# Kernel optimization log

Hardware: AMD Instinct MI355X
Metric: run time of the kernel (lower is better)

## Reference

```python
import math
import jax, jax.numpy as jnp
import numpy as np

B, S, H = 2, 2048, 1024
NH = 16
HD = H // NH            # 64
ROT = int(HD * 0.25)    # 16
QKV_SLOTS = 1024
PROJ_SLOTS = 1024
FFN_SLOTS = 4096
EPS = 1e-5


def gelu_l2_norm(x, axis=-1):
    # F.gelu (exact erf) then L2-normalize and rescale by sqrt(dim)
    g = jax.nn.gelu(x, approximate=False)
    n = jnp.linalg.norm(g, ord=2, axis=axis, keepdims=True)
    return g / n * math.sqrt(g.shape[axis])


def layer_norm(x, w, b):
    mu = jnp.mean(x, axis=-1, keepdims=True)
    var = jnp.mean(jnp.square(x - mu), axis=-1, keepdims=True)
    return (x - mu) * jax.lax.rsqrt(var + EPS) * w + b


def pattention(x, key_tok, val_tok):
    # [.., in] @ [slots, in]^T -> [.., slots]; NOTE: scale MULTIPLIES (as in source)
    aw = jnp.einsum('bsh,ph->bsp', x, key_tok) * math.sqrt(x.shape[-1])
    aw = gelu_l2_norm(aw, axis=-1)
    return jnp.einsum('bsp,pd->bsd', aw, val_tok)


def rotary_cos_sin(seq_len, rot_dim, base=10000.0):
    inv_freq = 1.0 / (base ** (jnp.arange(0, rot_dim, 2, dtype=jnp.float32) / rot_dim))
    t = jnp.arange(seq_len, dtype=jnp.float32)
    freqs = jnp.einsum('s,d->sd', t, inv_freq)           # [S, rot/2]
    emb = jnp.concatenate([freqs, freqs], axis=-1)       # [S, rot]
    return jnp.cos(emb), jnp.sin(emb)


def rotate_half(x):
    x1, x2 = jnp.split(x, 2, axis=-1)
    return jnp.concatenate([-x2, x1], axis=-1)


def setup_inputs() -> dict:
    key = jax.random.key(0)
    ks = jax.random.split(key, 12)
    p = lambda k, shape: jax.random.normal(k, shape, dtype=jnp.float32) * 0.02
    return {
        'x': jax.random.normal(ks[0], (B, S, H), dtype=jnp.float32),
        'ln1_w': jnp.ones((H,), jnp.float32), 'ln1_b': jnp.zeros((H,), jnp.float32),
        'ln2_w': jnp.ones((H,), jnp.float32), 'ln2_b': jnp.zeros((H,), jnp.float32),
        'q_key': p(ks[1], (QKV_SLOTS, H)), 'q_val': p(ks[2], (QKV_SLOTS, H)),
        'k_key': p(ks[3], (QKV_SLOTS, H)), 'k_val': p(ks[4], (QKV_SLOTS, H)),
        'v_key': p(ks[5], (QKV_SLOTS, H)), 'v_val': p(ks[6], (QKV_SLOTS, H)),
        'proj_key': p(ks[7], (PROJ_SLOTS, H)), 'proj_val': p(ks[8], (PROJ_SLOTS, H)),
        'ffn_key': p(ks[9], (FFN_SLOTS, H)), 'ffn_val': p(ks[10], (FFN_SLOTS, H)),
    }


def reference(x, ln1_w, ln1_b, ln2_w, ln2_b, q_key, q_val, k_key, k_val,
              v_key, v_val, proj_key, proj_val, ffn_key, ffn_val):
    residual = x
    xn = layer_norm(x, ln1_w, ln1_b)
    q = pattention(xn, q_key, q_val).reshape(B, S, NH, HD)
    k = pattention(xn, k_key, k_val).reshape(B, S, NH, HD)
    v = pattention(xn, v_key, v_val).reshape(B, S, NH, HD)

    cos, sin = rotary_cos_sin(S, ROT)          # [S, ROT]
    cos = cos[None, :, None, :]
    sin = sin[None, :, None, :]
    q_rot, q_pass = q[..., :ROT], q[..., ROT:]
    k_rot, k_pass = k[..., :ROT], k[..., ROT:]
    q_rot = q_rot * cos + rotate_half(q_rot) * sin
    k_rot = k_rot * cos + rotate_half(k_rot) * sin
    q = jnp.concatenate([q_rot, q_pass], axis=-1).transpose(0, 2, 1, 3)  # [B,NH,S,HD]
    k = jnp.concatenate([k_rot, k_pass], axis=-1).transpose(0, 2, 1, 3)
    v = v.transpose(0, 2, 1, 3)

    scale = math.sqrt(HD)
    causal = jnp.triu(jnp.ones((S, S), dtype=bool), k=1)
    attn_mask = jnp.where(causal, jnp.float32(-10000.0), jnp.float32(0.0))
    aw = jnp.einsum('bhqd,bhkd->bhqk', q, k) / scale + attn_mask
    aw = gelu_l2_norm(aw, axis=-1)
    o = jnp.einsum('bhqk,bhkd->bhqd', aw, v)
    o = o.transpose(0, 2, 1, 3).reshape(B, S, H)

    x = residual + pattention(o, proj_key, proj_val)
    residual = x
    x = residual + pattention(layer_norm(x, ln2_w, ln2_b), ffn_key, ffn_val)
    return x
```

## Files before the change

### kernel.cpp

```cpp
#include <hip/hip_runtime.h>

typedef __bf16 bf16x8 __attribute__((ext_vector_type(8)));
typedef float f32x4 __attribute__((ext_vector_type(4)));
typedef unsigned short u16;

__device__ __forceinline__ float b2f(u16 u) {
  union { unsigned int i; float f; } v; v.i = ((unsigned int)u) << 16; return v.f;
}
__device__ __forceinline__ u16 f2b(float f) {
  union { float f; unsigned int i; } v; v.f = f;
  unsigned int x = v.i;
  x += 0x7fffu + ((x >> 16) & 1u);
  return (u16)(x >> 16);
}
__device__ __forceinline__ float gelu_f(float x) {
  float x2 = x * x;
  float p = x * (2.3022083f + 0.1029434f * x2);
  float e = __builtin_amdgcn_exp2f(p);
  float r = __builtin_amdgcn_rcpf(1.0f + e);
  return x - x * r;
}
__device__ __forceinline__ void async16(const u16* g, u16* l) {
  __builtin_amdgcn_global_load_lds(
      (const __attribute__((address_space(1))) void*)g,
      (__attribute__((address_space(3))) void*)l, 16, 0, 0);
}
__device__ __forceinline__ void swz(int& bn, int& bm, int& bz) {
  int gx = (int)gridDim.x, gy = (int)gridDim.y;
  int flat = (int)(blockIdx.x + gridDim.x * (blockIdx.y + gridDim.y * blockIdx.z));
  int seq = flat >> 3;
  int nbm = gy >> 3;
  bm = (flat & 7) * nbm + seq % nbm;
  int rest = seq / nbm;
  bn = rest % gx;
  bz = rest / gx;
}

union U4 { uint4 u; u16 s[8]; };

__global__ __launch_bounds__(256) void prep_kernel(
    const float* __restrict__ qk, const float* __restrict__ kk,
    const float* __restrict__ vk, const float* __restrict__ pk,
    const float* __restrict__ fk, u16* __restrict__ w, float* __restrict__ ssqz,
    const float* __restrict__ qv, const float* __restrict__ kv,
    const float* __restrict__ vv, const float* __restrict__ pv,
    const float* __restrict__ fv, u16* __restrict__ valsT, u16* __restrict__ fvT,
    const float* __restrict__ x, const float* __restrict__ lnw,
    const float* __restrict__ lnb, u16* __restrict__ xn) {
  __shared__ float t[32][33];
  int id = (int)blockIdx.x;
  int tid = threadIdx.x;
  if (id < 9216) {
    int z = id >> 10;
    int i = (id & 1023) * 256 + tid;
    if (z == 8) {
      if (i < 20480) ssqz[i] = 0.f;
      return;
    }
    const float* in = (z == 0) ? qk : (z == 1) ? kk : (z == 2) ? vk : (z == 3) ? pk
                      : fk + (size_t)(z - 4) * 1048576;
    u16* o = w + (size_t)z * 1048576;
    float4 f = ((const float4*)in)[i];
    ushort4 s;
    s.x = f2b(f.x); s.y = f2b(f.y); s.z = f2b(f.z); s.w = f2b(f.w);
    ((ushort4*)o)[i] = s;
  } else if (id < 17408) {
    int rid = id - 9216;
    int bc = rid & 31, br = (rid >> 5) & 31, z = rid >> 10;
    const float* in; u16* o; int Rout, rowoff;
    if (z < 4) {
      in = (z == 0) ? qv : (z == 1) ? kv : (z == 2) ? vv : pv;
      o = valsT + (size_t)z * 1048576; Rout = 1024; rowoff = 0;
    } else {
      in = fv + (size_t)(z - 4) * 1048576;
      o = fvT; Rout = 4096; rowoff = (z - 4) * 1024;
    }
    int r = tid >> 5, cc = tid & 31;
    #pragma unroll
    for (int i = 0; i < 4; ++i)
      t[r + i * 8][cc] = in[(size_t)(br * 32 + r + i * 8) * 1024 + bc * 32 + cc];
    __syncthreads();
    #pragma unroll
    for (int i = 0; i < 4; ++i)
      o[(size_t)(bc * 32 + r + i * 8) * Rout + rowoff + br * 32 + cc] = f2b(t[cc][r + i * 8]);
  } else {
    int wv = tid >> 6, lane = tid & 63;
    int row = (id - 17408) * 4 + wv;
    const float* xr = x + (size_t)row * 1024;
    float4 v[4];
    float s = 0.f, s2 = 0.f;
    #pragma unroll
    for (int i = 0; i < 4; ++i) {
      v[i] = ((const float4*)xr)[lane + 64 * i];
      s += v[i].x + v[i].y + v[i].z + v[i].w;
      s2 += v[i].x * v[i].x + v[i].y * v[i].y + v[i].z * v[i].z + v[i].w * v[i].w;
    }
    #pragma unroll
    for (int m = 1; m < 64; m <<= 1) { s += __shfl_xor(s, m); s2 += __shfl_xor(s2, m); }
    float mu = s * (1.0f / 1024.0f);
    float inv = rsqrtf(s2 * (1.0f / 1024.0f) - mu * mu + 1e-5f);
    u16* orow = xn + (size_t)row * 1024;
    #pragma unroll
    for (int i = 0; i < 4; ++i) {
      int c = (lane + 64 * i) * 4;
      ushort4 o;
      o.x = f2b((v[i].x - mu) * inv * lnw[c]     + lnb[c]);
      o.y = f2b((v[i].y - mu) * inv * lnw[c + 1] + lnb[c + 1]);
      o.z = f2b((v[i].z - mu) * inv * lnw[c + 2] + lnb[c + 2]);
      o.w = f2b((v[i].w - mu) * inv * lnw[c + 3] + lnb[c + 3]);
      ((ushort4*)orow)[lane + 64 * i] = o;
    }
  }
}

__global__ __launch_bounds__(256) void ln_kernel(const float* __restrict__ x,
    const float* __restrict__ w, const float* __restrict__ b, u16* __restrict__ out) {
  int wv = threadIdx.x >> 6, lane = threadIdx.x & 63;
  int row = blockIdx.x * 4 + wv;
  const float* xr = x + (size_t)row * 1024;
  float4 v[4];
  float s = 0.f, s2 = 0.f;
  #pragma unroll
  for (int i = 0; i < 4; ++i) {
    v[i] = ((const float4*)xr)[lane + 64 * i];
    s += v[i].x + v[i].y + v[i].z + v[i].w;
    s2 += v[i].x * v[i].x + v[i].y * v[i].y + v[i].z * v[i].z + v[i].w * v[i].w;
  }
  #pragma unroll
  for (int m = 1; m < 64; m <<= 1) { s += __shfl_xor(s, m); s2 += __shfl_xor(s2, m); }
  float mu = s * (1.0f / 1024.0f);
  float inv = rsqrtf(s2 * (1.0f / 1024.0f) - mu * mu + 1e-5f);
  u16* orow = out + (size_t)row * 1024;
  #pragma unroll
  for (int i = 0; i < 4; ++i) {
    int c = (lane + 64 * i) * 4;
    ushort4 o;
    o.x = f2b((v[i].x - mu) * inv * w[c]     + b[c]);
    o.y = f2b((v[i].y - mu) * inv * w[c + 1] + b[c + 1]);
    o.z = f2b((v[i].z - mu) * inv * w[c + 2] + b[c + 2]);
    o.w = f2b((v[i].w - mu) * inv * w[c + 3] + b[c + 3]);
    ((ushort4*)orow)[lane + 64 * i] = o;
  }
}

template <int TM>
__global__ __launch_bounds__(256) void gemm_key(
    const u16* __restrict__ A, size_t sAz,
    const u16* __restrict__ B, size_t sBz,
    u16* __restrict__ C, size_t sCz,
    float* __restrict__ ssqb, size_t sSz,
    int N, int K, float alpha) {
  constexpr int AI = TM / 32;
  constexpr int G = TM / 64 + 2;
  __shared__ __align__(16) u16 As[3][TM * 32];
  __shared__ __align__(16) u16 Bs[3][128 * 32];
  int bn, bm, bz;
  swz(bn, bm, bz);
  const u16* Ab = A + (size_t)bz * sAz + (size_t)bm * TM * K;
  const u16* Bb = B + (size_t)bz * sBz + (size_t)bn * 128 * K;
  int tid = threadIdx.x, lane = tid & 63, wv = tid >> 6;
  int quad = lane >> 4, l16 = lane & 15;
  int lr = lane >> 2;
  int lcs = ((lane & 3) ^ ((lane >> 3) & 3)) * 8;
  int rq = quad ^ ((l16 >> 1) & 3);
  int wm = wv >> 1, wn = wv & 1;
  int RB = wm * (TM / 2), CB = wn * 64;
  auto STAGE = [&](int k0, int buf) {
    #pragma unroll
    for (int t = 0; t < TM / 64; ++t) {
      int ia = wv * (TM / 64) + t;
      async16(Ab + (size_t)(ia * 16 + lr) * K + k0 + lcs, &As[buf][ia * 512]);
    }
    #pragma unroll
    for (int t = 0; t < 2; ++t) {
      int ib = wv * 2 + t;
      async16(Bb + (size_t)(ib * 16 + lr) * K + k0 + lcs, &Bs[buf][ib * 512]);
    }
  };
  f32x4 zero = {0.f, 0.f, 0.f, 0.f};
  f32x4 acc[AI][4];
  #pragma unroll
  for (int i = 0; i < AI; ++i)
    #pragma unroll
    for (int j = 0; j < 4; ++j) acc[i][j] = zero;
  int NT = K >> 5;
  STAGE(0, 0);
  STAGE(32, 1);
  int cur = 0;
  for (int t = 0; t < NT; ++t) {
    if (t + 1 < NT) asm volatile("s_waitcnt vmcnt(%0)" :: "i"(G) : "memory");
    else            asm volatile("s_waitcnt vmcnt(0)" ::: "memory");
    __builtin_amdgcn_s_barrier();
    __builtin_amdgcn_sched_barrier(0);
    bf16x8 af[AI], bf[4];
    #pragma unroll
    for (int i = 0; i < AI; ++i)
      af[i] = *(const bf16x8*)&As[cur][(RB + i * 16 + l16) * 32 + rq * 8];
    #pragma unroll
    for (int j = 0; j < 4; ++j)
      bf[j] = *(const bf16x8*)&Bs[cur][(CB + j * 16 + l16) * 32 + rq * 8];
    if (t + 2 < NT) {
      int nb = cur + 2; if (nb >= 3) nb -= 3;
      STAGE((t + 2) * 32, nb);
    }
    #pragma unroll
    for (int i = 0; i < AI; ++i)
      #pragma unroll
      for (int j = 0; j < 4; ++j)
        acc[i][j] = __builtin_amdgcn_mfma_f32_16x16x32_bf16(af[i], bf[j], acc[i][j], 0, 0, 0);
    cur = (cur == 2) ? 0 : cur + 1;
  }
  #pragma unroll
  for (int i = 0; i < AI; ++i) {
    int rbase = bm * TM + RB + i * 16 + quad * 4;
    float srow[4] = {0.f, 0.f, 0.f, 0.f};
    #pragma unroll
    for (int j = 0; j < 4; ++j) {
      int c = bn * 128 + CB + j * 16 + l16;
      #pragma unroll
      for (int reg = 0; reg < 4; ++reg) {
        float g = gelu_f(acc[i][j][reg] * alpha);
        srow[reg] += g * g;
        C[(size_t)bz * sCz + (size_t)(rbase + reg) * N + c] = f2b(g);
      }
    }
    #pragma unroll
    for (int reg = 0; reg < 4; ++reg) {
      float s = srow[reg];
      s += __shfl_xor(s, 1); s += __shfl_xor(s, 2);
      s += __shfl_xor(s, 4); s += __shfl_xor(s, 8);
      if (l16 == 0) atomicAdd(&ssqb[bz * sSz + rbase + reg], s);
    }
  }
}

__global__ __launch_bounds__(256, 2) void gemm_fkey(
    const u16* __restrict__ A,
    const u16* __restrict__ B,
    u16* __restrict__ C,
    float* __restrict__ ssqb,
    int N, int K, float alpha) {
  __shared__ __align__(16) u16 As[2][128 * 32];
  __shared__ __align__(16) u16 Bs[3][256 * 32];
  int bn, bm, bz;
  swz(bn, bm, bz);
  const u16* Ab = A + (size_t)bm * 128 * K;
  const u16* Bb = B + (size_t)bn * 256 * K;
  int tid = threadIdx.x, lane = tid & 63, wv = tid >> 6;
  int quad = lane >> 4, l16 = lane & 15;
  int lr = lane >> 2;
  int lcs = ((lane & 3) ^ ((lane >> 3) & 3)) * 8;
  int rq = quad ^ ((l16 >> 1) & 3);
  int wm = wv >> 1, wn = wv & 1;
  int RB = wm * 64, CB = wn * 128;
  auto STAGE_A = [&](int k0, int buf) {
    #pragma unroll
    for (int t = 0; t < 2; ++t) {
      int ia = wv * 2 + t;
      async16(Ab + (size_t)(ia * 16 + lr) * K + k0 + lcs, &As[buf][ia * 512]);
    }
  };
  auto STAGE_B = [&](int k0, int buf) {
    #pragma unroll
    for (int t = 0; t < 4; ++t) {
      int ib = wv * 4 + t;
      async16(Bb + (size_t)(ib * 16 + lr) * K + k0 + lcs, &Bs[buf][ib * 512]);
    }
  };
  f32x4 zero = {0.f, 0.f, 0.f, 0.f};
  f32x4 acc[4][8];
  #pragma unroll
  for (int i = 0; i < 4; ++i)
    #pragma unroll
    for (int j = 0; j < 8; ++j) acc[i][j] = zero;
  int NT = K >> 5;
  STAGE_A(0, 0);
  STAGE_B(0, 0);
  STAGE_B(32, 1);
  int cb = 0;
  for (int t = 0; t < NT; ++t) {
    if (t + 1 < NT) asm volatile("s_waitcnt vmcnt(4)" ::: "memory");
    else            asm volatile("s_waitcnt vmcnt(0)" ::: "memory");
    __builtin_amdgcn_s_barrier();
    __builtin_amdgcn_sched_barrier(0);
    bf16x8 af[4], bf[8];
    #pragma unroll
    for (int i = 0; i < 4; ++i)
      af[i] = *(const bf16x8*)&As[t & 1][(RB + i * 16 + l16) * 32 + rq * 8];
    #pragma unroll
    for (int j = 0; j < 8; ++j)
      bf[j] = *(const bf16x8*)&Bs[cb][(CB + j * 16 + l16) * 32 + rq * 8];
    if (t + 1 < NT) STAGE_A((t + 1) * 32, (t + 1) & 1);
    if (t + 2 < NT) {
      int nb = cb + 2; if (nb >= 3) nb -= 3;
      STAGE_B((t + 2) * 32, nb);
    }
    #pragma unroll
    for (int i = 0; i < 4; ++i)
      #pragma unroll
      for (int j = 0; j < 8; ++j)
        acc[i][j] = __builtin_amdgcn_mfma_f32_16x16x32_bf16(af[i], bf[j], acc[i][j], 0, 0, 0);
    cb = (cb == 2) ? 0 : cb + 1;
  }
  #pragma unroll
  for (int i = 0; i < 4; ++i) {
    int rbase = bm * 128 + RB + i * 16 + quad * 4;
    float srow[4] = {0.f, 0.f, 0.f, 0.f};
    #pragma unroll
    for (int j = 0; j < 8; ++j) {
      int c = bn * 256 + CB + j * 16 + l16;
      #pragma unroll
      for (int reg = 0; reg < 4; ++reg) {
        float g = gelu_f(acc[i][j][reg] * alpha);
        srow[reg] += g * g;
        C[(size_t)(rbase + reg) * N + c] = f2b(g);
      }
    }
    #pragma unroll
    for (int reg = 0; reg < 4; ++reg) {
      float s = srow[reg];
      s += __shfl_xor(s, 1); s += __shfl_xor(s, 2);
      s += __shfl_xor(s, 4); s += __shfl_xor(s, 8);
      if (l16 == 0) atomicAdd(&ssqb[rbase + reg], s);
    }
  }
}

template <int TM, int MODE, bool ROT>
__global__ __launch_bounds__(256) void gemm_val(
    const u16* __restrict__ A, size_t sAz,
    const u16* __restrict__ B, size_t sBz,
    void* __restrict__ C, size_t sCz,
    const float* __restrict__ ssqb, size_t sSz,
    int N, int K, int kzs, int klen, float sqrtP, const float* __restrict__ res) {
  constexpr int AI = TM / 32;
  constexpr int G = TM / 64 + 2;
  __shared__ __align__(16) u16 As[3][TM * 32];
  __shared__ __align__(16) u16 Bs[3][128 * 32];
  int bn, bm, bz;
  swz(bn, bm, bz);
  const u16* Ab = A + (size_t)bz * sAz + (size_t)bm * TM * K;
  const u16* Bb = B + (size_t)bz * sBz + (size_t)bn * 128 * K;
  int tid = threadIdx.x, lane = tid & 63, wv = tid >> 6;
  int quad = lane >> 4, l16 = lane & 15;
  int lr = lane >> 2;
  int lcs = ((lane & 3) ^ ((lane >> 3) & 3)) * 8;
  int rq = quad ^ ((l16 >> 1) & 3);
  int wm = wv >> 1, wn = wv & 1;
  int RB = wm * (TM / 2), CB = wn * 64;
  int kb0 = bz * kzs;
  auto STAGE = [&](int k0, int buf) {
    #pragma unroll
    for (int t = 0; t < TM / 64; ++t) {
      int ia = wv * (TM / 64) + t;
      async16(Ab + (size_t)(ia * 16 + lr) * K + kb0 + k0 + lcs, &As[buf][ia * 512]);
    }
    #pragma unroll
    for (int t = 0; t < 2; ++t) {
      int ib = wv * 2 + t;
      async16(Bb + (size_t)(ib * 16 + lr) * K + kb0 + k0 + lcs, &Bs[buf][ib * 512]);
    }
  };
  f32x4 zero = {0.f, 0.f, 0.f, 0.f};
  f32x4 acc[AI][4];
  #pragma unroll
  for (int i = 0; i < AI; ++i)
    #pragma unroll
    for (int j = 0; j < 4; ++j) acc[i][j] = zero;
  int NT = klen >> 5;
  STAGE(0, 0);
  STAGE(32, 1);
  int cur = 0;
  for (int t = 0; t < NT; ++t) {
    if (t + 1 < NT) asm volatile("s_waitcnt vmcnt(%0)" :: "i"(G) : "memory");
    else            asm volatile("s_waitcnt vmcnt(0)" ::: "memory");
    __builtin_amdgcn_s_barrier();
    __builtin_amdgcn_sched_barrier(0);
    bf16x8 af[AI], bf[4];
    #pragma unroll
    for (int i = 0; i < AI; ++i)
      af[i] = *(const bf16x8*)&As[cur][(RB + i * 16 + l16) * 32 + rq * 8];
    #pragma unroll
    for (int j = 0; j < 4; ++j)
      bf[j] = *(const bf16x8*)&Bs[cur][(CB + j * 16 + l16) * 32 + rq * 8];
    if (t + 2 < NT) {
      int nb = cur + 2; if (nb >= 3) nb -= 3;
      STAGE((t + 2) * 32, nb);
    }
    #pragma unroll
    for (int i = 0; i < AI; ++i)
      #pragma unroll
      for (int j = 0; j < 4; ++j)
        acc[i][j] = __builtin_amdgcn_mfma_f32_16x16x32_bf16(af[i], bf[j], acc[i][j], 0, 0, 0);
    cur = (cur == 2) ? 0 : cur + 1;
  }
  #pragma unroll
  for (int i = 0; i < AI; ++i) {
    int rbase = bm * TM + RB + i * 16 + quad * 4;
    float sc[4];
    if (MODE < 2) {
      #pragma unroll
      for (int reg = 0; reg < 4; ++reg)
        sc[reg] = sqrtP * rsqrtf(ssqb[bz * sSz + rbase + reg]);
    }
    #pragma unroll
    for (int j = 0; j < 4; ++j) {
      int c = bn * 128 + CB + j * 16 + l16;
      #pragma unroll
      for (int reg = 0; reg < 4; ++reg) {
        float v = acc[i][j][reg];
        size_t idx = (size_t)(rbase + reg) * N + c;
        if (MODE == 0) {
          float vs = v * sc[reg];
          if (ROT && j == 0) {
            float prt = __shfl_xor(vs, 8);
            if (bz < 2) {
              int seq = (rbase + reg) & 2047;
              float fr = exp2f((float)(l16 & 7) * -1.66096404744368f);
              float ang = (float)seq * fr;
              float c_ = __cosf(ang), s_ = __sinf(ang);
              vs = (l16 < 8) ? (vs * c_ - prt * s_) : (vs * c_ + prt * s_);
            }
          }
          ((u16*)C)[(size_t)bz * sCz + idx] = f2b(vs);
        } else if (MODE == 1) {
          ((float*)C)[idx] = v * sc[reg] + res[idx];
        } else {
          ((float*)C)[(size_t)bz * sCz + idx] = v;
        }
      }
    }
  }
}

__global__ __launch_bounds__(256) void vt_kernel(const u16* __restrict__ vb,
                                                 u16* __restrict__ vT) {
  __shared__ __align__(16) u16 T[64][72];
  int st = blockIdx.x, bh = blockIdx.y;
  int b = bh >> 4, h = bh & 15;
  int tid = threadIdx.x;
  #pragma unroll
  for (int i = 0; i < 2; ++i) {
    int l = tid + 256 * i;
    int s = l >> 3, dc = l & 7;
    *(uint4*)&T[s][dc * 8] =
        *(const uint4*)(vb + (size_t)(b * 2048 + st * 64 + s) * 1024 + h * 64 + dc * 8);
  }
  __syncthreads();
  #pragma unroll
  for (int i = 0; i < 2; ++i) {
    int l = tid + 256 * i;
    int d = l >> 3, scid = l & 7;
    int blk = (scid >> 2) * 32;
    int qq = (scid & 3) * 4;
    U4 u;
    #pragma unroll
    for (int j = 0; j < 8; ++j)
      u.s[j] = T[blk + (j >> 2) * 16 + qq + (j & 3)][d];
    *(uint4*)(vT + ((size_t)bh * 64 + d) * 2048 + st * 64 + scid * 8) = u.u;
  }
}

__global__ __launch_bounds__(256) void attn_kernel(
    const u16* __restrict__ qb, const u16* __restrict__ kbp,
    const u16* __restrict__ vT, u16* __restrict__ ob,
    float* __restrict__ pP, float* __restrict__ ssqP) {
  __shared__ __align__(16) u16 Qs[64 * 64];
  __shared__ __align__(16) u16 Ks[2][64 * 64];
  __shared__ __align__(16) u16 Vts[2][64 * 64];
  int bh = blockIdx.x;
  int y = (int)blockIdx.y;
  int qt, kb, ke, half = 0;
  bool part = false;
  if (y == 0) { qt = 16; kb = 0; ke = 17; }
  else if (y <= 30) {
    int s = y - 1;
    qt = 31 - (s >> 1); half = s & 1; part = true;
    int n = qt + 1, h = (n + 1) >> 1;
    kb = half ? h : 0; ke = half ? n : h;
  } else { qt = 46 - y; kb = 0; ke = qt + 1; }
  int b = bh >> 4, h16 = bh & 15;
  const u16* qp = qb + (size_t)b * 2048 * 1024 + h16 * 64;
  const u16* kp = kbp + (size_t)b * 2048 * 1024 + h16 * 64;
  const u16* vp = vT + (size_t)bh * 64 * 2048;
  int tid = threadIdx.x, lane = tid & 63, wv = tid >> 6;
  int quad = lane >> 4, l16 = lane & 15;
  int lr8 = lane >> 3;
  int lc8s = ((lane & 7) ^ lr8) * 8;
  int rx = (l16 & 7) << 3;
  int MR = wv * 16;
  #pragma unroll
  for (int t = 0; t < 2; ++t) {
    int idx = wv * 2 + t;
    async16(qp + (size_t)(qt * 64 + idx * 8 + lr8) * 1024 + lc8s, &Qs[idx * 512]);
    async16(kp + (size_t)(kb * 64 + idx * 8 + lr8) * 1024 + lc8s, &Ks[0][idx * 512]);
    async16(vp + (size_t)(idx * 8 + lr8) * 2048 + kb * 64 + lc8s, &Vts[0][idx * 512]);
  }
  f32x4 zero = {0.f, 0.f, 0.f, 0.f};
  f32x4 oacc[4];
  #pragma unroll
  for (int dn = 0; dn < 4; ++dn) oacc[dn] = zero;
  float ssql = 0.f;
  bf16x8 bq0 = {}, bq1 = {};
  for (int kt = kb, cur = 0; kt < ke; ++kt, cur ^= 1) {
    __syncthreads();
    if (kt == kb) {
      bq0 = *(const bf16x8*)&Qs[((MR + l16) * 64 + quad * 8) ^ rx];
      bq1 = *(const bf16x8*)&Qs[((MR + l16) * 64 + 32 + quad * 8) ^ rx];
    }
    if (kt + 1 < ke) {
      #pragma unroll
      for (int t = 0; t < 2; ++t) {
        int idx = wv * 2 + t;
        async16(kp + (size_t)((kt + 1) * 64 + idx * 8 + lr8) * 1024 + lc8s, &Ks[cur ^ 1][idx * 512]);
        async16(vp + (size_t)(idx * 8 + lr8) * 2048 + (kt + 1) * 64 + lc8s, &Vts[cur ^ 1][idx * 512]);
      }
    }
    bool dg = (kt == qt);
    #pragma unroll
    for (int kc = 0; kc < 2; ++kc) {
      bf16x8 pf;
      #pragma unroll
      for (int snh = 0; snh < 2; ++snh) {
        int sn = kc * 2 + snh;
        bf16x8 ak0 = *(const bf16x8*)&Ks[cur][((sn * 16 + l16) * 64 + quad * 8) ^ rx];
        bf16x8 ak1 = *(const bf16x8*)&Ks[cur][((sn * 16 + l16) * 64 + 32 + quad * 8) ^ rx];
        f32x4 st = zero;
        st = __builtin_amdgcn_mfma_f32_16x16x32_bf16(ak0, bq0, st, 0, 0, 0);
        st = __builtin_amdgcn_mfma_f32_16x16x32_bf16(ak1, bq1, st, 0, 0, 0);
        #pragma unroll
        for (int r = 0; r < 4; ++r) {
          float gl = gelu_f(st[r] * 0.125f);
          if (dg && (sn * 16 + quad * 4 + r > MR + l16)) gl = 0.f;
          ssql += gl * gl;
          pf[snh * 4 + r] = (__bf16)gl;
        }
      }
      #pragma unroll
      for (int dn = 0; dn < 4; ++dn) {
        bf16x8 bv = *(const bf16x8*)&Vts[cur][((dn * 16 + l16) * 64 + kc * 32 + quad * 8) ^ rx];
        oacc[dn] = __builtin_amdgcn_mfma_f32_16x16x32_bf16(pf, bv, oacc[dn], 0, 0, 0);
      }
    }
  }
  ssql += __shfl_xor(ssql, 16);
  ssql += __shfl_xor(ssql, 32);
  if (!part) {
    float sc = 45.254834f * rsqrtf(ssql);
    #pragma unroll
    for (int dn = 0; dn < 4; ++dn)
      #pragma unroll
      for (int r = 0; r < 4; ++r) {
        float scr = __shfl(sc, quad * 4 + r);
        int row = qt * 64 + MR + quad * 4 + r;
        int col = h16 * 64 + dn * 16 + l16;
        ob[(size_t)(b * 2048 + row) * 1024 + col] = f2b(oacc[dn][r] * scr);
      }
  } else {
    int sp = ((qt - 17) * 32 + bh) * 2 + half;
    if (lane < 16) ssqP[sp * 64 + MR + l16] = ssql;
    float* po = pP + (size_t)sp * 4096;
    #pragma unroll
    for (int dn = 0; dn < 4; ++dn)
      #pragma unroll
      for (int r = 0; r < 4; ++r)
        po[(MR + quad * 4 + r) * 64 + dn * 16 + l16] = oacc[dn][r];
  }
}

__global__ __launch_bounds__(256) void acmb_kernel(
    const float* __restrict__ pP, const float* __restrict__ ssqP,
    u16* __restrict__ ob) {
  int s = blockIdx.x;
  int qt = 17 + (s >> 5), bh = s & 31;
  int b = bh >> 4, h = bh & 15;
  const float* p0 = pP + (size_t)(2 * s) * 4096;
  const float* p1 = p0 + 4096;
  int tid = threadIdx.x;
  int row = tid >> 2, c0 = (tid & 3) * 16;
  float sc = 45.254834f * rsqrtf(ssqP[(2 * s) * 64 + row] + ssqP[(2 * s + 1) * 64 + row]);
  u16* orow = ob + (size_t)(b * 2048 + qt * 64 + row) * 1024 + h * 64 + c0;
  #pragma unroll
  for (int i = 0; i < 16; i += 4) {
    float4 a = *(const float4*)(p0 + row * 64 + c0 + i);
    float4 c = *(const float4*)(p1 + row * 64 + c0 + i);
    ushort4 o;
    o.x = f2b((a.x + c.x) * sc); o.y = f2b((a.y + c.y) * sc);
    o.z = f2b((a.z + c.z) * sc); o.w = f2b((a.w + c.w) * sc);
    *(ushort4*)(orow + i) = o;
  }
}

__global__ __launch_bounds__(256) void fin_kernel(
    const float* __restrict__ p0, const float* __restrict__ p1,
    const float* __restrict__ x1, const float* __restrict__ ssqf,
    float* __restrict__ out) {
  int row = blockIdx.x, t = threadIdx.x;
  float s = 64.0f * rsqrtf(ssqf[row]);
  size_t base = (size_t)row * 1024 + t * 4;
  float4 a = *(const float4*)(p0 + base);
  float4 b = *(const float4*)(p1 + base);
  float4 r = *(const float4*)(x1 + base);
  float4 o;
  o.x = r.x + s * (a.x + b.x); o.y = r.y + s * (a.y + b.y);
  o.z = r.z + s * (a.z + b.z); o.w = r.w + s * (a.w + b.w);
  *(float4*)(out + base) = o;
}

extern "C" void kernel_launch(void* const* d_in, const int* in_sizes, int n_in,
                              void* d_out, int out_size, void* d_ws, size_t ws_size,
                              hipStream_t stream) {
  const float* x    = (const float*)d_in[0];
  const float* ln1w = (const float*)d_in[1];
  const float* ln1b = (const float*)d_in[2];
  const float* ln2w = (const float*)d_in[3];
  const float* ln2b = (const float*)d_in[4];
  const float* qk   = (const float*)d_in[5];
  const float* qv   = (const float*)d_in[6];
  const float* kk   = (const float*)d_in[7];
  const float* kv   = (const float*)d_in[8];
  const float* vk   = (const float*)d_in[9];
  const float* vv   = (const float*)d_in[10];
  const float* pk   = (const float*)d_in[11];
  const float* pv   = (const float*)d_in[12];
  const float* fk   = (const float*)d_in[13];
  const float* fv   = (const float*)d_in[14];
  float* out = (float*)d_out;

  const size_t M1 = 1048576;
  u16* w = (u16*)d_ws;
  u16* wkeys  = w;
  u16* wpk    = w + 3 * M1;
  u16* wfk    = w + 4 * M1;
  u16* wvalsT = w + 8 * M1;
  u16* wpvT   = w + 11 * M1;
  u16* wfvT   = w + 12 * M1;
  u16* xn     = w + 16 * M1;
  u16* gq     = w + 20 * M1;
  u16* ob     = w + 20 * M1;
  u16* vT     = w + 24 * M1;
  u16* gp     = w + 28 * M1;
  u16* gf     = w + 20 * M1;
  u16* qb     = w + 36 * M1;
  u16* kb     = w + 40 * M1;
  u16* vb     = w + 44 * M1;
  float* ssq_qkv  = (float*)(w + 48 * M1);
  float* ssq_proj = ssq_qkv + 12288;
  float* ssq_ffn  = ssq_qkv + 16384;
  float* x1 = (float*)(w + 52 * M1);
  float* p0 = (float*)w;
  float* p1 = (float*)(w + 36 * M1);
  float* pP   = (float*)(w + 28 * M1);
  float* ssqP = (float*)(w + 52 * M1);

  dim3 blk(256);
  prep_kernel<<<18432, blk, 0, stream>>>(
      qk, kk, vk, pk, fk, w, ssq_qkv,
      qv, kv, vv, pv, fv, wvalsT, wfvT,
      x, ln1w, ln1b, xn);

  gemm_key<128><<<dim3(8, 32, 3), blk, 0, stream>>>(
      xn, 0, wkeys, M1, gq, 4 * M1, ssq_qkv, 4096, 1024, 1024, 32.0f);
  gemm_val<128, 0, true><<<dim3(8, 32, 3), blk, 0, stream>>>(
      gq, 4 * M1, wvalsT, M1, qb, 4 * M1, ssq_qkv, 4096, 1024, 1024, 0, 1024, 32.0f, nullptr);

  vt_kernel<<<dim3(32, 32), blk, 0, stream>>>(vb, vT);
  attn_kernel<<<dim3(32, 47), blk, 0, stream>>>(qb, kb, vT, ob, pP, ssqP);
  acmb_kernel<<<480, blk, 0, stream>>>(pP, ssqP, ob);

  gemm_key<64><<<dim3(8, 64, 1), blk, 0, stream>>>(
      ob, 0, wpk, 0, gp, 0, ssq_proj, 0, 1024, 1024, 32.0f);
  gemm_val<64, 1, false><<<dim3(8, 64, 1), blk, 0, stream>>>(
      gp, 0, wpvT, 0, x1, 0, ssq_proj, 0, 1024, 1024, 0, 1024, 32.0f, x);

  ln_kernel<<<1024, blk, 0, stream>>>(x1, ln2w, ln2b, xn);
  gemm_fkey<<<dim3(16, 32, 1), blk, 0, stream>>>(
      xn, wfk, gf, ssq_ffn, 4096, 1024, 32.0f);
  gemm_val<128, 2, false><<<dim3(8, 32, 2), blk, 0, stream>>>(
      gf, 0, wfvT, 0, p0, 18 * M1, ssq_ffn, 0, 1024, 4096, 2048, 2048, 0.0f, nullptr);
  fin_kernel<<<4096, blk, 0, stream>>>(p0, p1, x1, ssq_ffn, out);
}
```

Before: 401.5 us.

## Add wide 128x256-tile value GEMM kernel for QKV and FFN value projections

Adds gemm_valw, a value-projection GEMM with 128x256 output tiles (each wave computes 64x128), double-buffered A and triple-buffered B staging, and launch bounds for two blocks per CU. The QKV and FFN value GEMMs switch to it, halving the grid along N. Larger tiles raise arithmetic intensity and reuse of A across more columns, cutting global and LDS traffic per MFMA. The cost is many more accumulator registers and fewer blocks, which may lower occupancy and wave-level parallelism. Rotary handling is moved into the new kernel and dropped from the old one, which now only serves the proj GEMM.

```diff
diff --git a/kernel.cpp b/kernel.cpp
--- a/kernel.cpp
+++ b/kernel.cpp
@@ -322,6 +322,113 @@
       s += __shfl_xor(s, 1); s += __shfl_xor(s, 2);
       s += __shfl_xor(s, 4); s += __shfl_xor(s, 8);
       if (l16 == 0) atomicAdd(&ssqb[rbase + reg], s);
+    }
+  }
+}
+
+template <int MODE, bool ROT>
+__global__ __launch_bounds__(256, 2) void gemm_valw(
+    const u16* __restrict__ A, size_t sAz,
+    const u16* __restrict__ B, size_t sBz,
+    void* __restrict__ C, size_t sCz,
+    const float* __restrict__ ssqb, size_t sSz,
+    int N, int K, int kzs, int klen, float sqrtP) {
+  __shared__ __align__(16) u16 As[2][128 * 32];
+  __shared__ __align__(16) u16 Bs[3][256 * 32];
+  int bn, bm, bz;
+  swz(bn, bm, bz);
+  const u16* Ab = A + (size_t)bz * sAz + (size_t)bm * 128 * K;
+  const u16* Bb = B + (size_t)bz * sBz + (size_t)bn * 256 * K;
+  int koff = bz * kzs;
+  int tid = threadIdx.x, lane = tid & 63, wv = tid >> 6;
+  int quad = lane >> 4, l16 = lane & 15;
+  int lr = lane >> 2;
+  int lcs = ((lane & 3) ^ ((lane >> 3) & 3)) * 8;
+  int rq = quad ^ ((l16 >> 1) & 3);
+  int wm = wv >> 1, wn = wv & 1;
+  int RB = wm * 64, CB = wn * 128;
+  auto STAGE_A = [&](int k0, int buf) {
+    #pragma unroll
+    for (int t = 0; t < 2; ++t) {
+      int ia = wv * 2 + t;
+      async16(Ab + (size_t)(ia * 16 + lr) * K + koff + k0 + lcs, &As[buf][ia * 512]);
+    }
+  };
+  auto STAGE_B = [&](int k0, int buf) {
+    #pragma unroll
+    for (int t = 0; t < 4; ++t) {
+      int ib = wv * 4 + t;
+      async16(Bb + (size_t)(ib * 16 + lr) * K + koff + k0 + lcs, &Bs[buf][ib * 512]);
+    }
+  };
+  f32x4 zero = {0.f, 0.f, 0.f, 0.f};
+  f32x4 acc[4][8];
+  #pragma unroll
+  for (int i = 0; i < 4; ++i)
+    #pragma unroll
+    for (int j = 0; j < 8; ++j) acc[i][j] = zero;
+  int NT = klen >> 5;
+  STAGE_A(0, 0);
+  STAGE_B(0, 0);
+  STAGE_B(32, 1);
+  int cb = 0;
+  for (int t = 0; t < NT; ++t) {
+    if (t + 1 < NT) asm volatile("s_waitcnt vmcnt(4)" ::: "memory");
+    else            asm volatile("s_waitcnt vmcnt(0)" ::: "memory");
+    __builtin_amdgcn_s_barrier();
+    __builtin_amdgcn_sched_barrier(0);
+    bf16x8 af[4], bf[8];
+    #pragma unroll
+    for (int i = 0; i < 4; ++i)
+      af[i] = *(const bf16x8*)&As[t & 1][(RB + i * 16 + l16) * 32 + rq * 8];
+    #pragma unroll
+    for (int j = 0; j < 8; ++j)
+      bf[j] = *(const bf16x8*)&Bs[cb][(CB + j * 16 + l16) * 32 + rq * 8];
+    if (t + 1 < NT) STAGE_A((t + 1) * 32, (t + 1) & 1);
+    if (t + 2 < NT) {
+      int nb = cb + 2; if (nb >= 3) nb -= 3;
+      STAGE_B((t + 2) * 32, nb);
+    }
+    #pragma unroll
+    for (int i = 0; i < 4; ++i)
+      #pragma unroll
+      for (int j = 0; j < 8; ++j)
+        acc[i][j] = __builtin_amdgcn_mfma_f32_16x16x32_bf16(af[i], bf[j], acc[i][j], 0, 0, 0);
+    cb = (cb == 2) ? 0 : cb + 1;
+  }
+  #pragma unroll
+  for (int i = 0; i < 4; ++i) {
+    int rbase = bm * 128 + RB + i * 16 + quad * 4;
+    float sc[4];
+    if (MODE == 0) {
+      #pragma unroll
+      for (int reg = 0; reg < 4; ++reg)
+        sc[reg] = sqrtP * rsqrtf(ssqb[bz * sSz + rbase + reg]);
+    }
+    #pragma unroll
+    for (int j = 0; j < 8; ++j) {
+      int c = bn * 256 + CB + j * 16 + l16;
+      #pragma unroll
+      for (int reg = 0; reg < 4; ++reg) {
+        float v = acc[i][j][reg];
+        size_t idx = (size_t)(rbase + reg) * N + c;
+        if (MODE == 0) {
+          float vs = v * sc[reg];
+          if (ROT && (j & 3) == 0) {
+            float prt = __shfl_xor(vs, 8);
+            if (bz < 2) {
+              int seq = (rbase + reg) & 2047;
+              float fr = exp2f((float)(l16 & 7) * -1.66096404744368f);
+              float ang = (float)seq * fr;
+              float c_ = __cosf(ang), s_ = __sinf(ang);
+              vs = (l16 < 8) ? (vs * c_ - prt * s_) : (vs * c_ + prt * s_);
+            }
+          }
+          ((u16*)C)[(size_t)bz * sCz + idx] = f2b(vs);
+        } else {
+          ((float*)C)[(size_t)bz * sCz + idx] = v;
+        }
+      }
     }
   }
 }
@@ -411,18 +518,7 @@
         float v = acc[i][j][reg];
         size_t idx = (size_t)(rbase + reg) * N + c;
         if (MODE == 0) {
-          float vs = v * sc[reg];
-          if (ROT && j == 0) {
-            float prt = __shfl_xor(vs, 8);
-            if (bz < 2) {
-              int seq = (rbase + reg) & 2047;
-              float fr = exp2f((float)(l16 & 7) * -1.66096404744368f);
-              float ang = (float)seq * fr;
-              float c_ = __cosf(ang), s_ = __sinf(ang);
-              vs = (l16 < 8) ? (vs * c_ - prt * s_) : (vs * c_ + prt * s_);
-            }
-          }
-          ((u16*)C)[(size_t)bz * sCz + idx] = f2b(vs);
+          ((u16*)C)[(size_t)bz * sCz + idx] = f2b(v * sc[reg]);
         } else if (MODE == 1) {
           ((float*)C)[idx] = v * sc[reg] + res[idx];
         } else {
@@ -661,8 +757,8 @@
 
   gemm_key<128><<<dim3(8, 32, 3), blk, 0, stream>>>(
       xn, 0, wkeys, M1, gq, 4 * M1, ssq_qkv, 4096, 1024, 1024, 32.0f);
-  gemm_val<128, 0, true><<<dim3(8, 32, 3), blk, 0, stream>>>(
-      gq, 4 * M1, wvalsT, M1, qb, 4 * M1, ssq_qkv, 4096, 1024, 1024, 0, 1024, 32.0f, nullptr);
+  gemm_valw<0, true><<<dim3(4, 32, 3), blk, 0, stream>>>(
+      gq, 4 * M1, wvalsT, M1, qb, 4 * M1, ssq_qkv, 4096, 1024, 1024, 0, 1024, 32.0f);
 
   vt_kernel<<<dim3(32, 32), blk, 0, stream>>>(vb, vT);
   attn_kernel<<<dim3(32, 47), blk, 0, stream>>>(qb, kb, vT, ob, pP, ssqP);
@@ -676,7 +772,7 @@
   ln_kernel<<<1024, blk, 0, stream>>>(x1, ln2w, ln2b, xn);
   gemm_fkey<<<dim3(16, 32, 1), blk, 0, stream>>>(
       xn, wfk, gf, ssq_ffn, 4096, 1024, 32.0f);
-  gemm_val<128, 2, false><<<dim3(8, 32, 2), blk, 0, stream>>>(
-      gf, 0, wfvT, 0, p0, 18 * M1, ssq_ffn, 0, 1024, 4096, 2048, 2048, 0.0f, nullptr);
+  gemm_valw<2, false><<<dim3(4, 32, 2), blk, 0, stream>>>(
+      gf, 0, wfvT, 0, (u16*)p0, 18 * M1, ssq_ffn, 0, 1024, 4096, 2048, 2048, 0.0f);
   fin_kernel<<<4096, blk, 0, stream>>>(p0, p1, x1, ssq_ffn, out);
 }
```

Measured after the change: 407.9 us. No clear change (+1.6%).
